# Performance work log

Hardware: AMD Instinct MI355X
Metric: run time of the kernel (lower is better)

The kernel has to match this reference:

```python
import jax, jax.numpy as jnp
import numpy as np

SEGMENT_LENGTHS = [1024, 2048, 4096]
DILATION_RATES = [1, 2, 4]


def setup_inputs() -> dict:
    key = jax.random.key(0)
    k1, k2, k3 = jax.random.split(key, 3)
    n = sum(SEGMENT_LENGTHS)  # 7168
    shape = (1, n, 8, 64)  # (b, n, h, d)
    q = jax.random.normal(k1, shape, dtype=jnp.float32)
    k = jax.random.normal(k2, shape, dtype=jnp.float32)
    v = jax.random.normal(k3, shape, dtype=jnp.float32)
    return {"q": q, "k": k, "v": v}


def _attend(q_seg, k_kv, v_kv):
    # q_seg: [b, q_len, h, d]; k_kv/v_kv: [b, k_len, h, d]
    d = q_seg.shape[-1]
    scale = 1.0 / jnp.sqrt(jnp.asarray(d, q_seg.dtype))
    scores = jnp.einsum("bqhd,bkhd->bhqk", q_seg, k_kv) * scale
    w = jax.nn.softmax(scores, axis=-1)
    return jnp.einsum("bhqk,bkhd->bqhd", w, v_kv)


def reference(q, k, v):
    # Single-device dilated attention (ring_size == 1, is_causal=False).
    n = q.shape[1]
    output = jnp.zeros_like(q)
    seg_start = 0
    for seg_len, dilation in zip(SEGMENT_LENGTHS, DILATION_RATES):
        if seg_start >= n:
            break
        seg_end = min(seg_start + seg_len, n)
        q_seg = q[:, seg_start:seg_end]
        if dilation > 1:
            k_d = k[:, ::dilation]
            v_d = v[:, ::dilation]
        else:
            k_d, v_d = k, v
        out_seg = _attend(q_seg, k_d, v_d)
        output = output.at[:, seg_start:seg_end].set(out_seg)
        seg_start = seg_end
    return output
```

## Files before the change

kernel.cpp:

```cpp
#include <hip/hip_runtime.h>

#define VB0 3670016L
#define VB1 7340032L
#define VB2 9175040L
#define PO_OFF 5046272L
#define PL_OFF (PO_OFF + 512L * 128 * 64)

typedef short bvec8 __attribute__((ext_vector_type(8)));
typedef float fvec16 __attribute__((ext_vector_type(16)));

static __device__ __forceinline__ short f2bf(float f) {
  unsigned u = __float_as_uint(f);
  u = u + 0x7fffu + ((u >> 16) & 1u);
  return (short)(u >> 16);
}

#if defined(__has_builtin)
#if __has_builtin(__builtin_amdgcn_cvt_pk_bf16_f32)
#define HAVE_CVTPK 1
#endif
#if __has_builtin(__builtin_amdgcn_permlane32_swap)
#define HAVE_PLSWAP 1
#endif
#endif

static __device__ __forceinline__ unsigned pk2(float a, float b) {
#ifdef HAVE_CVTPK
  auto r = __builtin_amdgcn_cvt_pk_bf16_f32(a, b);
  unsigned u; __builtin_memcpy(&u, &r, 4);
  return u;
#else
  unsigned ua = (__float_as_uint(a) + 0x8000u) >> 16;
  unsigned ub = (__float_as_uint(b) + 0x8000u) & 0xffff0000u;
  return ua | ub;
#endif
}
static __device__ __forceinline__ void async16(const short* g, short* l) {
  __builtin_amdgcn_global_load_lds((const __attribute__((address_space(1))) unsigned*)(void*)g,
                                   (__attribute__((address_space(3))) unsigned*)(void*)l, 16, 0, 0);
}

__global__ __launch_bounds__(256) void pack_all(const float* __restrict__ k,
                                                const float* __restrict__ v,
                                                short* __restrict__ W) {
  __shared__ float tl[64][65];
  int b = blockIdx.x, t = threadIdx.x;
  if (b < 896) {
    int h = b / 112, tile = b % 112, i0 = tile * 64;
    int r = t >> 2, c = t & 3;
    const float* src = k + ((long)(i0 + r) * 8 + h) * 64 + c * 16;
    short* dst = W + ((long)h * 7168 + i0 + r) * 64 + c * 16;
    union { unsigned u[8]; bvec8 v[2]; } tw;
#pragma unroll
    for (int q4 = 0; q4 < 4; q4++) {
      float4 x = *(const float4*)(src + q4 * 4);
      tw.u[q4 * 2 + 0] = pk2(x.x, x.y);
      tw.u[q4 * 2 + 1] = pk2(x.z, x.w);
    }
    *(bvec8*)dst = tw.v[0];
    *(bvec8*)(dst + 8) = tw.v[1];
  } else {
    int b2 = b - 896;
    int h, tile, dil, L; long base;
    if (b2 < 896)       { L = 7168; dil = 1; h = b2 / 112; tile = b2 % 112; base = VB0; }
    else if (b2 < 1344) { int bb = b2 - 896;  L = 3584; dil = 2; h = bb / 56; tile = bb % 56; base = VB1; }
    else                { int bb = b2 - 1344; L = 1792; dil = 4; h = bb / 28; tile = bb % 28; base = VB2; }
    int i0 = tile * 64;
    int row = t >> 2, c = t & 3;
    const float* src = v + ((long)(i0 + row) * dil * 8 + h) * 64;
#pragma unroll
    for (int cc = 0; cc < 4; cc++) {
      int d0 = c * 16 + cc * 4;
      float4 x = *(const float4*)(src + d0);
      tl[row][d0 + 0] = x.x; tl[row][d0 + 1] = x.y;
      tl[row][d0 + 2] = x.z; tl[row][d0 + 3] = x.w;
    }
    __syncthreads();
    int d = t >> 2, part = t & 3;
    union { unsigned u[8]; bvec8 v[2]; } tw;
#pragma unroll
    for (int u2 = 0; u2 < 8; u2++)
      tw.u[u2] = pk2(tl[part * 16 + 2 * u2][d], tl[part * 16 + 2 * u2 + 1][d]);
    short* dst = W + base + ((long)h * 64 + d) * L + i0 + part * 16;
    *(bvec8*)dst = tw.v[0];
    *(bvec8*)(dst + 8) = tw.v[1];
  }
}

__global__ __launch_bounds__(256, 3) void attn_kern(const float* __restrict__ q,
                                                    const short* __restrict__ W,
                                                    float* __restrict__ out,
                                                    float* __restrict__ PO,
                                                    float* __restrict__ PL) {
  int b = blockIdx.x;
  int h, q0, dil, kt0, L; long vbo;
  if (b < 256)      { int sp = b & 3; h = (b >> 2) & 7; int qt = b >> 5;
                      q0 = qt * 128;        dil = 1; L = 7168; vbo = VB0; kt0 = sp * 28; }
  else if (b < 512) { int i = b - 256; int sp = i & 1; h = (i >> 1) & 7; int qt = i >> 4;
                      q0 = 1024 + qt * 128; dil = 2; L = 3584; vbo = VB1; kt0 = sp * 28; }
  else              { int i = b - 512; h = i & 7; int qt = i >> 3;
                      q0 = 3072 + qt * 128; dil = 4; L = 1792; vbo = VB2; kt0 = 0; }
  const short* kb = W + (long)h * 7168 * 64;
  const short* vt = W + vbo + (long)h * 64 * L;
  const int dil64 = dil * 64;

  __shared__ __attribute__((aligned(16))) short sK[3][4096];
  __shared__ __attribute__((aligned(16))) short sV[3][4096];
  short* sKf = &sK[0][0];
  short* sVf = &sV[0][0];

  int t = threadIdx.x, lane = t & 63, w = t >> 6;
  int ln = lane & 31, hb = lane >> 5;

  bvec8 qb[4];
  {
    const float* qp = q + ((long)(q0 + w * 32 + ln) * 8 + h) * 64 + 8 * hb;
    const float qs = 0.125f * 1.44269504088896f;
#pragma unroll
    for (int ks = 0; ks < 4; ks++) {
      union { unsigned u[4]; bvec8 v; } qu;
#pragma unroll
      for (int jj = 0; jj < 4; jj++)
        qu.u[jj] = pk2(qs * qp[ks * 16 + 2 * jj], qs * qp[ks * 16 + 2 * jj + 1]);
      qb[ks] = qu.v;
    }
  }

  bvec8 onesf;
#pragma unroll
  for (int j = 0; j < 8; j++) onesf[j] = (short)0x3F80;

  int srow = lane >> 3, sch = (lane & 7) ^ srow;
  const long kstep = 64L * dil64;
  const short* gk0; const short* gk1; const short* gv0; const short* gv1;
  {
    int row0 = (w * 2 + 0) * 8 + srow, row1 = (w * 2 + 1) * 8 + srow;
    long kb0 = (long)kt0 * 64;
    gk0 = kb + (kb0 + row0) * dil64 + sch * 8;
    gk1 = kb + (kb0 + row1) * dil64 + sch * 8;
    gv0 = vt + (long)row0 * L + kb0 + sch * 8;
    gv1 = vt + (long)row1 * L + kb0 + sch * 8;
  }
  const int ldoff = w * 2 * 512;
  auto stage = [&](int bo) {
    async16(gk0, sKf + bo + ldoff);
    async16(gv0, sVf + bo + ldoff);
    async16(gk1, sKf + bo + ldoff + 512);
    async16(gv1, sVf + bo + ldoff + 512);
    gk0 += kstep; gk1 += kstep; gv0 += 64; gv1 += 64;
  };

  stage(0);
  stage(4096);

  int koff[8];
#pragma unroll
  for (int ks = 0; ks < 4; ks++)
#pragma unroll
    for (int mb = 0; mb < 2; mb++)
      koff[ks * 2 + mb] = (mb * 32 + ln) * 64 + (((2 * ks + hb) ^ (ln & 7)) * 8);

  fvec16 Oa[2], La;
#pragma unroll
  for (int i = 0; i < 16; i++) { Oa[0][i] = 0.f; Oa[1][i] = 0.f; La[i] = 0.f; }

  int bo = 0;
  int bs = 8192;
  for (int it = 0; it < 28; it++) {
    if (it < 27) asm volatile("s_waitcnt vmcnt(4)" ::: "memory");
    else         asm volatile("s_waitcnt vmcnt(0)" ::: "memory");
    __builtin_amdgcn_s_barrier();
    asm volatile("" ::: "memory");

    if (it < 26) { stage(bs); bs = (bs == 8192) ? 0 : bs + 4096; }

    const short* sb   = sKf + bo;
    const short* vbuf = sVf + bo;
    bo = (bo == 8192) ? 0 : bo + 4096;

    bvec8 vf[8];
#pragma unroll
    for (int ks = 0; ks < 4; ks++)
#pragma unroll
      for (int mb = 0; mb < 2; mb++)
        vf[mb * 4 + ks] = *(const bvec8*)(vbuf + koff[ks * 2 + mb]);

    fvec16 Sa[2];
#pragma unroll
    for (int i = 0; i < 16; i++) { Sa[0][i] = 0.f; Sa[1][i] = 0.f; }
    __builtin_amdgcn_s_setprio(1);
#pragma unroll
    for (int ks = 0; ks < 4; ks++)
#pragma unroll
      for (int mb = 0; mb < 2; mb++) {
        bvec8 kf = *(const bvec8*)(sb + koff[ks * 2 + mb]);
        Sa[mb] = __builtin_amdgcn_mfma_f32_32x32x16_bf16(kf, qb[ks], Sa[mb], 0, 0, 0);
      }
    __builtin_amdgcn_s_setprio(0);

#pragma unroll
    for (int ks2 = 0; ks2 < 4; ks2++) {
      int mb = ks2 >> 1, r0i = (ks2 & 1) * 8;
      float p[8];
#pragma unroll
      for (int u = 0; u < 8; u++)
        p[u] = __builtin_amdgcn_exp2f(Sa[mb][r0i + u]);
      unsigned da0 = pk2(p[0], p[1]), da1 = pk2(p[2], p[3]);
      unsigned db0 = pk2(p[4], p[5]), db1 = pk2(p[6], p[7]);
      union { unsigned u[4]; bvec8 v; } fu;
#ifdef HAVE_PLSWAP
      {
        auto rr0 = __builtin_amdgcn_permlane32_swap((int)da0, (int)db0, false, false);
        auto rr1 = __builtin_amdgcn_permlane32_swap((int)da1, (int)db1, false, false);
        __builtin_memcpy(&fu.u[0], &rr0, 4);
        __builtin_memcpy(&fu.u[2], (const char*)&rr0 + 4, 4);
        __builtin_memcpy(&fu.u[1], &rr1, 4);
        __builtin_memcpy(&fu.u[3], (const char*)&rr1 + 4, 4);
      }
#else
      unsigned s0 = hb ? da0 : db0, s1 = hb ? da1 : db1;
      unsigned x0 = __shfl_xor(s0, 32), x1 = __shfl_xor(s1, 32);
      fu.u[0] = hb ? x0 : da0;  fu.u[1] = hb ? x1 : da1;
      fu.u[2] = hb ? db0 : x0;  fu.u[3] = hb ? db1 : x1;
#endif
      __builtin_amdgcn_s_setprio(1);
      Oa[0] = __builtin_amdgcn_mfma_f32_32x32x16_bf16(vf[ks2], fu.v, Oa[0], 0, 0, 0);
      Oa[1] = __builtin_amdgcn_mfma_f32_32x32x16_bf16(vf[4 + ks2], fu.v, Oa[1], 0, 0, 0);
      La    = __builtin_amdgcn_mfma_f32_32x32x16_bf16(onesf, fu.v, La, 0, 0, 0);
      __builtin_amdgcn_s_setprio(0);
    }
  }

  float lf = La[0];
  int wl = w * 32 + ln;
  if (b < 512) {
    float* po = PO + ((long)b * 128 + wl) * 64;
#pragma unroll
    for (int mb2 = 0; mb2 < 2; mb2++)
#pragma unroll
      for (int r2 = 0; r2 < 4; r2++) {
        float4 x = { Oa[mb2][r2 * 4 + 0], Oa[mb2][r2 * 4 + 1],
                     Oa[mb2][r2 * 4 + 2], Oa[mb2][r2 * 4 + 3] };
        *(float4*)(po + mb2 * 32 + r2 * 8 + hb * 4) = x;
      }
    if (hb == 0) PL[(long)b * 128 + wl] = lf;
  } else {
    float inv = 1.f / lf;
    float* op = out + ((long)(q0 + wl) * 8 + h) * 64;
#pragma unroll
    for (int mb2 = 0; mb2 < 2; mb2++)
#pragma unroll
      for (int r2 = 0; r2 < 4; r2++) {
        float4 x = { Oa[mb2][r2 * 4 + 0] * inv, Oa[mb2][r2 * 4 + 1] * inv,
                     Oa[mb2][r2 * 4 + 2] * inv, Oa[mb2][r2 * 4 + 3] * inv };
        *(float4*)(op + mb2 * 32 + r2 * 8 + hb * 4) = x;
      }
  }
}

__global__ __launch_bounds__(256) void combine_kern(const float* __restrict__ PO,
                                                    const float* __restrict__ PL,
                                                    float* __restrict__ out) {
  int g = blockIdx.x, t = threadIdx.x;
  int base_b, nsp, q0, h;
  if (g < 64) { int qt = g >> 3; h = g & 7; base_b = qt * 32 + h * 4; nsp = 4; q0 = qt * 128; }
  else { int gi = g - 64; int qt = gi >> 3; h = gi & 7; base_b = 256 + qt * 16 + h * 2; nsp = 2; q0 = 1024 + qt * 128; }
  int r = t >> 1, ch = (t & 1) * 32;
  float lt = 0.f;
  for (int sp = 0; sp < nsp; sp++) lt += PL[(long)(base_b + sp) * 128 + r];
  float inv = 1.f / lt;
  float4 acc[8];
#pragma unroll
  for (int j = 0; j < 8; j++) { acc[j].x = 0.f; acc[j].y = 0.f; acc[j].z = 0.f; acc[j].w = 0.f; }
  for (int sp = 0; sp < nsp; sp++) {
    const float4* pb = (const float4*)(PO + ((long)(base_b + sp) * 128 + r) * 64 + ch);
#pragma unroll
    for (int j = 0; j < 8; j++) {
      float4 x = pb[j];
      acc[j].x += x.x; acc[j].y += x.y; acc[j].z += x.z; acc[j].w += x.w;
    }
  }
  float4* op = (float4*)(out + ((long)(q0 + r) * 8 + h) * 64 + ch);
#pragma unroll
  for (int j = 0; j < 8; j++) {
    float4 x = { acc[j].x * inv, acc[j].y * inv, acc[j].z * inv, acc[j].w * inv };
    op[j] = x;
  }
}

extern "C" void kernel_launch(void* const* d_in, const int* in_sizes, int n_in,
                              void* d_out, int out_size, void* d_ws, size_t ws_size,
                              hipStream_t stream) {
  const float* q = (const float*)d_in[0];
  const float* k = (const float*)d_in[1];
  const float* v = (const float*)d_in[2];
  float* out = (float*)d_out;
  short* W = (short*)d_ws;
  float* PO = (float*)d_ws + PO_OFF;
  float* PL = (float*)d_ws + PL_OFF;

  pack_all<<<2464, 256, 0, stream>>>(k, v, W);
  attn_kern<<<768, 256, 0, stream>>>(q, W, out, PO, PL);
  combine_kern<<<192, 256, 0, stream>>>(PO, PL, out);
}
```

Baseline: 159.5 us.

## Split key tile across wave pairs with two query tiles per wave and LDS reduction

Each wave now owns two 32-row query tiles and half of each 64-key tile, so every K fragment read from LDS feeds two MFMAs. Partial outputs from the two key halves are combined through shared memory at the end. The row-sum MFMA against a ones vector is replaced by scalar adds of the exponentials, and the triple-buffered async staging becomes double-buffered with a full __syncthreads each iteration. This trades fewer LDS reads and MFMAs for more accumulator registers, an extra cross-wave reduction, and less load/compute overlap.

```diff
diff --git a/kernel.cpp b/kernel.cpp
--- a/kernel.cpp
+++ b/kernel.cpp
@@ -104,31 +104,32 @@
   const short* vt = W + vbo + (long)h * 64 * L;
   const int dil64 = dil * 64;
 
-  __shared__ __attribute__((aligned(16))) short sK[3][4096];
-  __shared__ __attribute__((aligned(16))) short sV[3][4096];
+  __shared__ __attribute__((aligned(16))) short sK[2][4096];
+  __shared__ __attribute__((aligned(16))) short sV[2][4096];
+  __shared__ float sLm[2][2][64];
   short* sKf = &sK[0][0];
   short* sVf = &sV[0][0];
 
   int t = threadIdx.x, lane = t & 63, w = t >> 6;
   int ln = lane & 31, hb = lane >> 5;
-
-  bvec8 qb[4];
+  int kbh = w & 1, qh = w >> 1;
+
+  bvec8 qb[2][4];
   {
-    const float* qp = q + ((long)(q0 + w * 32 + ln) * 8 + h) * 64 + 8 * hb;
     const float qs = 0.125f * 1.44269504088896f;
 #pragma unroll
-    for (int ks = 0; ks < 4; ks++) {
-      union { unsigned u[4]; bvec8 v; } qu;
-#pragma unroll
-      for (int jj = 0; jj < 4; jj++)
-        qu.u[jj] = pk2(qs * qp[ks * 16 + 2 * jj], qs * qp[ks * 16 + 2 * jj + 1]);
-      qb[ks] = qu.v;
-    }
-  }
-
-  bvec8 onesf;
-#pragma unroll
-  for (int j = 0; j < 8; j++) onesf[j] = (short)0x3F80;
+    for (int jq = 0; jq < 2; jq++) {
+      const float* qp = q + ((long)(q0 + (qh * 2 + jq) * 32 + ln) * 8 + h) * 64 + 8 * hb;
+#pragma unroll
+      for (int ks = 0; ks < 4; ks++) {
+        union { unsigned u[4]; bvec8 v; } qu;
+#pragma unroll
+        for (int jj = 0; jj < 4; jj++)
+          qu.u[jj] = pk2(qs * qp[ks * 16 + 2 * jj], qs * qp[ks * 16 + 2 * jj + 1]);
+        qb[jq][ks] = qu.v;
+      }
+    }
+  }
 
   int srow = lane >> 3, sch = (lane & 7) ^ srow;
   const long kstep = 64L * dil64;
@@ -142,119 +143,153 @@
     gv1 = vt + (long)row1 * L + kb0 + sch * 8;
   }
   const int ldoff = w * 2 * 512;
-  auto stage = [&](int bo) {
-    async16(gk0, sKf + bo + ldoff);
-    async16(gv0, sVf + bo + ldoff);
-    async16(gk1, sKf + bo + ldoff + 512);
-    async16(gv1, sVf + bo + ldoff + 512);
+  auto stage = [&](int bo2) {
+    async16(gk0, sKf + bo2 + ldoff);
+    async16(gv0, sVf + bo2 + ldoff);
+    async16(gk1, sKf + bo2 + ldoff + 512);
+    async16(gv1, sVf + bo2 + ldoff + 512);
     gk0 += kstep; gk1 += kstep; gv0 += 64; gv1 += 64;
   };
 
   stage(0);
-  stage(4096);
-
-  int koff[8];
+
+  int koffK[4], koffV[4];
 #pragma unroll
   for (int ks = 0; ks < 4; ks++)
-#pragma unroll
-    for (int mb = 0; mb < 2; mb++)
-      koff[ks * 2 + mb] = (mb * 32 + ln) * 64 + (((2 * ks + hb) ^ (ln & 7)) * 8);
-
-  fvec16 Oa[2], La;
-#pragma unroll
-  for (int i = 0; i < 16; i++) { Oa[0][i] = 0.f; Oa[1][i] = 0.f; La[i] = 0.f; }
+    koffK[ks] = (kbh * 32 + ln) * 64 + (((2 * ks + hb) ^ (ln & 7)) * 8);
+#pragma unroll
+  for (int dh = 0; dh < 2; dh++)
+#pragma unroll
+    for (int sp = 0; sp < 2; sp++)
+      koffV[dh * 2 + sp] = (dh * 32 + ln) * 64 + (((2 * (2 * kbh + sp) + hb) ^ (ln & 7)) * 8);
+
+  fvec16 Oa[2][2];
+  float lacc[2] = {0.f, 0.f};
+#pragma unroll
+  for (int i = 0; i < 16; i++) { Oa[0][0][i] = 0.f; Oa[0][1][i] = 0.f; Oa[1][0][i] = 0.f; Oa[1][1][i] = 0.f; }
 
   int bo = 0;
-  int bs = 8192;
   for (int it = 0; it < 28; it++) {
-    if (it < 27) asm volatile("s_waitcnt vmcnt(4)" ::: "memory");
-    else         asm volatile("s_waitcnt vmcnt(0)" ::: "memory");
-    __builtin_amdgcn_s_barrier();
-    asm volatile("" ::: "memory");
-
-    if (it < 26) { stage(bs); bs = (bs == 8192) ? 0 : bs + 4096; }
-
-    const short* sb   = sKf + bo;
-    const short* vbuf = sVf + bo;
-    bo = (bo == 8192) ? 0 : bo + 4096;
-
-    bvec8 vf[8];
-#pragma unroll
-    for (int ks = 0; ks < 4; ks++)
-#pragma unroll
-      for (int mb = 0; mb < 2; mb++)
-        vf[mb * 4 + ks] = *(const bvec8*)(vbuf + koff[ks * 2 + mb]);
+    __syncthreads();
+    if (it < 27) stage(bo ^ 4096);
+
+    const short* sb = sKf + bo;
+    const short* vb = sVf + bo;
+    bo ^= 4096;
+
+    bvec8 vf[4];
+#pragma unroll
+    for (int i = 0; i < 4; i++) vf[i] = *(const bvec8*)(vb + koffV[i]);
 
     fvec16 Sa[2];
 #pragma unroll
     for (int i = 0; i < 16; i++) { Sa[0][i] = 0.f; Sa[1][i] = 0.f; }
     __builtin_amdgcn_s_setprio(1);
 #pragma unroll
-    for (int ks = 0; ks < 4; ks++)
-#pragma unroll
-      for (int mb = 0; mb < 2; mb++) {
-        bvec8 kf = *(const bvec8*)(sb + koff[ks * 2 + mb]);
-        Sa[mb] = __builtin_amdgcn_mfma_f32_32x32x16_bf16(kf, qb[ks], Sa[mb], 0, 0, 0);
+    for (int ks = 0; ks < 4; ks++) {
+      bvec8 kf = *(const bvec8*)(sb + koffK[ks]);
+      Sa[0] = __builtin_amdgcn_mfma_f32_32x32x16_bf16(kf, qb[0][ks], Sa[0], 0, 0, 0);
+      Sa[1] = __builtin_amdgcn_mfma_f32_32x32x16_bf16(kf, qb[1][ks], Sa[1], 0, 0, 0);
+    }
+    __builtin_amdgcn_s_setprio(0);
+
+#pragma unroll
+    for (int jq = 0; jq < 2; jq++)
+#pragma unroll
+      for (int sp = 0; sp < 2; sp++) {
+        int r0i = sp * 8;
+        float p[8];
+#pragma unroll
+        for (int u = 0; u < 8; u++)
+          p[u] = __builtin_amdgcn_exp2f(Sa[jq][r0i + u]);
+        lacc[jq] += ((p[0] + p[1]) + (p[2] + p[3])) + ((p[4] + p[5]) + (p[6] + p[7]));
+        unsigned da0 = pk2(p[0], p[1]), da1 = pk2(p[2], p[3]);
+        unsigned db0 = pk2(p[4], p[5]), db1 = pk2(p[6], p[7]);
+        union { unsigned u[4]; bvec8 v; } fu;
+#ifdef HAVE_PLSWAP
+        {
+          auto rr0 = __builtin_amdgcn_permlane32_swap((int)da0, (int)db0, false, false);
+          auto rr1 = __builtin_amdgcn_permlane32_swap((int)da1, (int)db1, false, false);
+          __builtin_memcpy(&fu.u[0], &rr0, 4);
+          __builtin_memcpy(&fu.u[2], (const char*)&rr0 + 4, 4);
+          __builtin_memcpy(&fu.u[1], &rr1, 4);
+          __builtin_memcpy(&fu.u[3], (const char*)&rr1 + 4, 4);
+        }
+#else
+        unsigned s0 = hb ? da0 : db0, s1 = hb ? da1 : db1;
+        unsigned x0 = __shfl_xor(s0, 32), x1 = __shfl_xor(s1, 32);
+        fu.u[0] = hb ? x0 : da0;  fu.u[1] = hb ? x1 : da1;
+        fu.u[2] = hb ? db0 : x0;  fu.u[3] = hb ? db1 : x1;
+#endif
+        __builtin_amdgcn_s_setprio(1);
+        Oa[jq][0] = __builtin_amdgcn_mfma_f32_32x32x16_bf16(vf[sp], fu.v, Oa[jq][0], 0, 0, 0);
+        Oa[jq][1] = __builtin_amdgcn_mfma_f32_32x32x16_bf16(vf[2 + sp], fu.v, Oa[jq][1], 0, 0, 0);
+        __builtin_amdgcn_s_setprio(0);
       }
-    __builtin_amdgcn_s_setprio(0);
-
-#pragma unroll
-    for (int ks2 = 0; ks2 < 4; ks2++) {
-      int mb = ks2 >> 1, r0i = (ks2 & 1) * 8;
-      float p[8];
-#pragma unroll
-      for (int u = 0; u < 8; u++)
-        p[u] = __builtin_amdgcn_exp2f(Sa[mb][r0i + u]);
-      unsigned da0 = pk2(p[0], p[1]), da1 = pk2(p[2], p[3]);
-      unsigned db0 = pk2(p[4], p[5]), db1 = pk2(p[6], p[7]);
-      union { unsigned u[4]; bvec8 v; } fu;
-#ifdef HAVE_PLSWAP
-      {
-        auto rr0 = __builtin_amdgcn_permlane32_swap((int)da0, (int)db0, false, false);
-        auto rr1 = __builtin_amdgcn_permlane32_swap((int)da1, (int)db1, false, false);
-        __builtin_memcpy(&fu.u[0], &rr0, 4);
-        __builtin_memcpy(&fu.u[2], (const char*)&rr0 + 4, 4);
-        __builtin_memcpy(&fu.u[1], &rr1, 4);
-        __builtin_memcpy(&fu.u[3], (const char*)&rr1 + 4, 4);
+  }
+
+  float lt[2];
+#pragma unroll
+  for (int jq = 0; jq < 2; jq++)
+    lt[jq] = lacc[jq] + __shfl_xor(lacc[jq], 32);
+
+  __syncthreads();
+  if (kbh) {
+    float* dst = qh ? (float*)sVf : (float*)sKf;
+#pragma unroll
+    for (int jq = 0; jq < 2; jq++)
+#pragma unroll
+      for (int dh = 0; dh < 2; dh++)
+#pragma unroll
+        for (int r = 0; r < 16; r++)
+          dst[((jq * 2 + dh) * 16 + r) * 64 + lane] = Oa[jq][dh][r];
+    sLm[qh][0][lane] = lt[0];
+    sLm[qh][1][lane] = lt[1];
+  }
+  __syncthreads();
+  if (!kbh) {
+    const float* src = qh ? (const float*)sVf : (const float*)sKf;
+#pragma unroll
+    for (int jq = 0; jq < 2; jq++)
+#pragma unroll
+      for (int dh = 0; dh < 2; dh++)
+#pragma unroll
+        for (int r = 0; r < 16; r++)
+          Oa[jq][dh][r] += src[((jq * 2 + dh) * 16 + r) * 64 + lane];
+    lt[0] += sLm[qh][0][lane];
+    lt[1] += sLm[qh][1][lane];
+
+    if (b < 512) {
+#pragma unroll
+      for (int jq = 0; jq < 2; jq++) {
+        int wl = (qh * 2 + jq) * 32 + ln;
+        float* po = PO + ((long)b * 128 + wl) * 64;
+#pragma unroll
+        for (int dh = 0; dh < 2; dh++)
+#pragma unroll
+          for (int r2 = 0; r2 < 4; r2++) {
+            float4 x = { Oa[jq][dh][r2 * 4 + 0], Oa[jq][dh][r2 * 4 + 1],
+                         Oa[jq][dh][r2 * 4 + 2], Oa[jq][dh][r2 * 4 + 3] };
+            *(float4*)(po + dh * 32 + r2 * 8 + hb * 4) = x;
+          }
+        if (hb == 0) PL[(long)b * 128 + wl] = lt[jq];
       }
-#else
-      unsigned s0 = hb ? da0 : db0, s1 = hb ? da1 : db1;
-      unsigned x0 = __shfl_xor(s0, 32), x1 = __shfl_xor(s1, 32);
-      fu.u[0] = hb ? x0 : da0;  fu.u[1] = hb ? x1 : da1;
-      fu.u[2] = hb ? db0 : x0;  fu.u[3] = hb ? db1 : x1;
-#endif
-      __builtin_amdgcn_s_setprio(1);
-      Oa[0] = __builtin_amdgcn_mfma_f32_32x32x16_bf16(vf[ks2], fu.v, Oa[0], 0, 0, 0);
-      Oa[1] = __builtin_amdgcn_mfma_f32_32x32x16_bf16(vf[4 + ks2], fu.v, Oa[1], 0, 0, 0);
-      La    = __builtin_amdgcn_mfma_f32_32x32x16_bf16(onesf, fu.v, La, 0, 0, 0);
-      __builtin_amdgcn_s_setprio(0);
-    }
-  }
-
-  float lf = La[0];
-  int wl = w * 32 + ln;
-  if (b < 512) {
-    float* po = PO + ((long)b * 128 + wl) * 64;
-#pragma unroll
-    for (int mb2 = 0; mb2 < 2; mb2++)
-#pragma unroll
-      for (int r2 = 0; r2 < 4; r2++) {
-        float4 x = { Oa[mb2][r2 * 4 + 0], Oa[mb2][r2 * 4 + 1],
-                     Oa[mb2][r2 * 4 + 2], Oa[mb2][r2 * 4 + 3] };
-        *(float4*)(po + mb2 * 32 + r2 * 8 + hb * 4) = x;
+    } else {
+#pragma unroll
+      for (int jq = 0; jq < 2; jq++) {
+        int wl = (qh * 2 + jq) * 32 + ln;
+        float inv = 1.f / lt[jq];
+        float* op = out + ((long)(q0 + wl) * 8 + h) * 64;
+#pragma unroll
+        for (int dh = 0; dh < 2; dh++)
+#pragma unroll
+          for (int r2 = 0; r2 < 4; r2++) {
+            float4 x = { Oa[jq][dh][r2 * 4 + 0] * inv, Oa[jq][dh][r2 * 4 + 1] * inv,
+                         Oa[jq][dh][r2 * 4 + 2] * inv, Oa[jq][dh][r2 * 4 + 3] * inv };
+            *(float4*)(op + dh * 32 + r2 * 8 + hb * 4) = x;
+          }
       }
-    if (hb == 0) PL[(long)b * 128 + wl] = lf;
-  } else {
-    float inv = 1.f / lf;
-    float* op = out + ((long)(q0 + wl) * 8 + h) * 64;
-#pragma unroll
-    for (int mb2 = 0; mb2 < 2; mb2++)
-#pragma unroll
-      for (int r2 = 0; r2 < 4; r2++) {
-        float4 x = { Oa[mb2][r2 * 4 + 0] * inv, Oa[mb2][r2 * 4 + 1] * inv,
-                     Oa[mb2][r2 * 4 + 2] * inv, Oa[mb2][r2 * 4 + 3] * inv };
-        *(float4*)(op + mb2 * 32 + r2 * 8 + hb * 4) = x;
-      }
+    }
   }
 }
 
```

Measured after the change: 176.7 us. 10.8% more time.

## Prefetch next K tile into registers mid-iteration and replace ones-MFMA row sum with VALU

Applied to the files above, without the earlier changes.

Restructures the main loop so the barrier and next-stage async copy sit in the middle of the softmax/PV work, and the next tile's K fragments are loaded from LDS into registers early so the QK MFMAs no longer wait on LDS reads. The row-sum MFMA against a ones vector is replaced by a scalar float accumulation of the exp values, combined across half-waves with a shuffle at the end. This cuts MFMA work per iteration and overlaps memory waits with compute, at the cost of more live registers (kf[8]) and a stricter vmcnt(0) wait each iteration. The row sum now uses the fp32 exp values instead of their bf16-rounded versions, which slightly changes the normalisation numerics.

```diff
diff --git a/kernel.cpp b/kernel.cpp
--- a/kernel.cpp
+++ b/kernel.cpp
@@ -8,12 +8,6 @@
 
 typedef short bvec8 __attribute__((ext_vector_type(8)));
 typedef float fvec16 __attribute__((ext_vector_type(16)));
-
-static __device__ __forceinline__ short f2bf(float f) {
-  unsigned u = __float_as_uint(f);
-  u = u + 0x7fffu + ((u >> 16) & 1u);
-  return (short)(u >> 16);
-}
 
 #if defined(__has_builtin)
 #if __has_builtin(__builtin_amdgcn_cvt_pk_bf16_f32)
@@ -86,6 +80,43 @@
     *(bvec8*)(dst + 8) = tw.v[1];
   }
 }
+
+#ifdef HAVE_PLSWAP
+#define PEXCH(fu, da0, da1, db0, db1)                                              \
+  do {                                                                             \
+    auto rr0 = __builtin_amdgcn_permlane32_swap((int)(da0), (int)(db0), false, false); \
+    auto rr1 = __builtin_amdgcn_permlane32_swap((int)(da1), (int)(db1), false, false); \
+    __builtin_memcpy(&fu.u4[0], &rr0, 4);                                          \
+    __builtin_memcpy(&fu.u4[2], (const char*)&rr0 + 4, 4);                         \
+    __builtin_memcpy(&fu.u4[1], &rr1, 4);                                          \
+    __builtin_memcpy(&fu.u4[3], (const char*)&rr1 + 4, 4);                         \
+  } while (0)
+#else
+#define PEXCH(fu, da0, da1, db0, db1)                                              \
+  do {                                                                             \
+    unsigned s0 = hb ? (da0) : (db0), s1 = hb ? (da1) : (db1);                     \
+    unsigned x0 = __shfl_xor(s0, 32), x1 = __shfl_xor(s1, 32);                     \
+    fu.u4[0] = hb ? x0 : (da0);  fu.u4[1] = hb ? x1 : (da1);                       \
+    fu.u4[2] = hb ? (db0) : x0;  fu.u4[3] = hb ? (db1) : x1;                       \
+  } while (0)
+#endif
+
+#define SOFTMAX_PV(KS2)                                                            \
+  do {                                                                             \
+    const int mb_ = (KS2) >> 1, r0_ = ((KS2) & 1) * 8;                             \
+    float p[8];                                                                    \
+    _Pragma("unroll") for (int u = 0; u < 8; u++)                                  \
+        p[u] = __builtin_amdgcn_exp2f(Sa[mb_][r0_ + u]);                           \
+    lacc += ((p[0] + p[1]) + (p[2] + p[3])) + ((p[4] + p[5]) + (p[6] + p[7]));     \
+    unsigned da0 = pk2(p[0], p[1]), da1 = pk2(p[2], p[3]);                         \
+    unsigned db0 = pk2(p[4], p[5]), db1 = pk2(p[6], p[7]);                         \
+    union { unsigned u4[4]; bvec8 v; } fu;                                         \
+    PEXCH(fu, da0, da1, db0, db1);                                                 \
+    __builtin_amdgcn_s_setprio(1);                                                 \
+    Oa[0] = __builtin_amdgcn_mfma_f32_32x32x16_bf16(vf[(KS2)], fu.v, Oa[0], 0, 0, 0);     \
+    Oa[1] = __builtin_amdgcn_mfma_f32_32x32x16_bf16(vf[4 + (KS2)], fu.v, Oa[1], 0, 0, 0); \
+    __builtin_amdgcn_s_setprio(0);                                                 \
+  } while (0)
 
 __global__ __launch_bounds__(256, 3) void attn_kern(const float* __restrict__ q,
                                                     const short* __restrict__ W,
@@ -126,10 +157,6 @@
     }
   }
 
-  bvec8 onesf;
-#pragma unroll
-  for (int j = 0; j < 8; j++) onesf[j] = (short)0x3F80;
-
   int srow = lane >> 3, sch = (lane & 7) ^ srow;
   const long kstep = 64L * dil64;
   const short* gk0; const short* gk1; const short* gv0; const short* gv1;
@@ -142,16 +169,19 @@
     gv1 = vt + (long)row1 * L + kb0 + sch * 8;
   }
   const int ldoff = w * 2 * 512;
-  auto stage = [&](int bo) {
-    async16(gk0, sKf + bo + ldoff);
-    async16(gv0, sVf + bo + ldoff);
-    async16(gk1, sKf + bo + ldoff + 512);
-    async16(gv1, sVf + bo + ldoff + 512);
+  auto stage = [&](int bo2) {
+    async16(gk0, sKf + bo2 + ldoff);
+    async16(gv0, sVf + bo2 + ldoff);
+    async16(gk1, sKf + bo2 + ldoff + 512);
+    async16(gv1, sVf + bo2 + ldoff + 512);
     gk0 += kstep; gk1 += kstep; gv0 += 64; gv1 += 64;
   };
 
   stage(0);
   stage(4096);
+  asm volatile("s_waitcnt vmcnt(4)" ::: "memory");
+  __builtin_amdgcn_s_barrier();
+  asm volatile("" ::: "memory");
 
   int koff[8];
 #pragma unroll
@@ -160,78 +190,55 @@
     for (int mb = 0; mb < 2; mb++)
       koff[ks * 2 + mb] = (mb * 32 + ln) * 64 + (((2 * ks + hb) ^ (ln & 7)) * 8);
 
-  fvec16 Oa[2], La;
-#pragma unroll
-  for (int i = 0; i < 16; i++) { Oa[0][i] = 0.f; Oa[1][i] = 0.f; La[i] = 0.f; }
-
-  int bo = 0;
-  int bs = 8192;
+  bvec8 kf[8];
+#pragma unroll
+  for (int i = 0; i < 8; i++) kf[i] = *(const bvec8*)(sKf + koff[i]);
+
+  fvec16 Oa[2];
+  float lacc = 0.f;
+#pragma unroll
+  for (int i = 0; i < 16; i++) { Oa[0][i] = 0.f; Oa[1][i] = 0.f; }
+
+  int bc = 0, bn = 4096, bs = 8192;
   for (int it = 0; it < 28; it++) {
-    if (it < 27) asm volatile("s_waitcnt vmcnt(4)" ::: "memory");
-    else         asm volatile("s_waitcnt vmcnt(0)" ::: "memory");
+    bvec8 vf[8];
+#pragma unroll
+    for (int ks = 0; ks < 4; ks++)
+#pragma unroll
+      for (int mb = 0; mb < 2; mb++)
+        vf[mb * 4 + ks] = *(const bvec8*)(sVf + bc + koff[ks * 2 + mb]);
+
+    fvec16 Sa[2];
+#pragma unroll
+    for (int i = 0; i < 16; i++) { Sa[0][i] = 0.f; Sa[1][i] = 0.f; }
+    __builtin_amdgcn_s_setprio(1);
+#pragma unroll
+    for (int ks = 0; ks < 4; ks++) {
+      Sa[0] = __builtin_amdgcn_mfma_f32_32x32x16_bf16(kf[ks * 2 + 0], qb[ks], Sa[0], 0, 0, 0);
+      Sa[1] = __builtin_amdgcn_mfma_f32_32x32x16_bf16(kf[ks * 2 + 1], qb[ks], Sa[1], 0, 0, 0);
+    }
+    __builtin_amdgcn_s_setprio(0);
+
+    SOFTMAX_PV(0);
+    SOFTMAX_PV(1);
+
+    asm volatile("s_waitcnt vmcnt(0)" ::: "memory");
     __builtin_amdgcn_s_barrier();
     asm volatile("" ::: "memory");
 
-    if (it < 26) { stage(bs); bs = (bs == 8192) ? 0 : bs + 4096; }
-
-    const short* sb   = sKf + bo;
-    const short* vbuf = sVf + bo;
-    bo = (bo == 8192) ? 0 : bo + 4096;
-
-    bvec8 vf[8];
-#pragma unroll
-    for (int ks = 0; ks < 4; ks++)
-#pragma unroll
-      for (int mb = 0; mb < 2; mb++)
-        vf[mb * 4 + ks] = *(const bvec8*)(vbuf + koff[ks * 2 + mb]);
-
-    fvec16 Sa[2];
-#pragma unroll
-    for (int i = 0; i < 16; i++) { Sa[0][i] = 0.f; Sa[1][i] = 0.f; }
-    __builtin_amdgcn_s_setprio(1);
-#pragma unroll
-    for (int ks = 0; ks < 4; ks++)
-#pragma unroll
-      for (int mb = 0; mb < 2; mb++) {
-        bvec8 kf = *(const bvec8*)(sb + koff[ks * 2 + mb]);
-        Sa[mb] = __builtin_amdgcn_mfma_f32_32x32x16_bf16(kf, qb[ks], Sa[mb], 0, 0, 0);
-      }
-    __builtin_amdgcn_s_setprio(0);
-
-#pragma unroll
-    for (int ks2 = 0; ks2 < 4; ks2++) {
-      int mb = ks2 >> 1, r0i = (ks2 & 1) * 8;
-      float p[8];
-#pragma unroll
-      for (int u = 0; u < 8; u++)
-        p[u] = __builtin_amdgcn_exp2f(Sa[mb][r0i + u]);
-      unsigned da0 = pk2(p[0], p[1]), da1 = pk2(p[2], p[3]);
-      unsigned db0 = pk2(p[4], p[5]), db1 = pk2(p[6], p[7]);
-      union { unsigned u[4]; bvec8 v; } fu;
-#ifdef HAVE_PLSWAP
-      {
-        auto rr0 = __builtin_amdgcn_permlane32_swap((int)da0, (int)db0, false, false);
-        auto rr1 = __builtin_amdgcn_permlane32_swap((int)da1, (int)db1, false, false);
-        __builtin_memcpy(&fu.u[0], &rr0, 4);
-        __builtin_memcpy(&fu.u[2], (const char*)&rr0 + 4, 4);
-        __builtin_memcpy(&fu.u[1], &rr1, 4);
-        __builtin_memcpy(&fu.u[3], (const char*)&rr1 + 4, 4);
-      }
-#else
-      unsigned s0 = hb ? da0 : db0, s1 = hb ? da1 : db1;
-      unsigned x0 = __shfl_xor(s0, 32), x1 = __shfl_xor(s1, 32);
-      fu.u[0] = hb ? x0 : da0;  fu.u[1] = hb ? x1 : da1;
-      fu.u[2] = hb ? db0 : x0;  fu.u[3] = hb ? db1 : x1;
-#endif
-      __builtin_amdgcn_s_setprio(1);
-      Oa[0] = __builtin_amdgcn_mfma_f32_32x32x16_bf16(vf[ks2], fu.v, Oa[0], 0, 0, 0);
-      Oa[1] = __builtin_amdgcn_mfma_f32_32x32x16_bf16(vf[4 + ks2], fu.v, Oa[1], 0, 0, 0);
-      La    = __builtin_amdgcn_mfma_f32_32x32x16_bf16(onesf, fu.v, La, 0, 0, 0);
-      __builtin_amdgcn_s_setprio(0);
-    }
-  }
-
-  float lf = La[0];
+    if (it < 26) stage(bs);
+    if (it < 27) {
+#pragma unroll
+      for (int i = 0; i < 8; i++) kf[i] = *(const bvec8*)(sKf + bn + koff[i]);
+    }
+
+    SOFTMAX_PV(2);
+    SOFTMAX_PV(3);
+
+    bc = bn; bn = bs; bs = (bs == 8192) ? 0 : bs + 4096;
+  }
+
+  float lf = lacc + __shfl_xor(lacc, 32);
   int wl = w * 32 + ln;
   if (b < 512) {
     float* po = PO + ((long)b * 128 + wl) * 64;
```

After: 156.2 us. -2.1%, faster.
